# Performance work log

Hardware: AMD Instinct MI355X
Metric: run time of the kernel (lower is better)

The kernel has to match this reference:

```python
import jax, jax.numpy as jnp
import numpy as np

N_QUBITS = 12
N_LAYERS = 4


def rot_mat(phi, theta, omega):
    # PennyLane Rot(phi,theta,omega) = RZ(omega) @ RY(theta) @ RZ(phi)
    c = jnp.cos(theta / 2).astype(jnp.complex64)
    s = jnp.sin(theta / 2).astype(jnp.complex64)
    ep = jnp.exp(-1j * (phi + omega) / 2).astype(jnp.complex64)
    em = jnp.exp(1j * (phi - omega) / 2).astype(jnp.complex64)
    return jnp.stack([
        jnp.stack([ep * c, -em * s]),
        jnp.stack([jnp.conj(em) * s, jnp.conj(ep) * c]),
    ])  # (2,2) complex64


def apply_1q(state, U, w):
    # state: (batch, 2, 2, ..., 2) with N_QUBITS qubit axes
    s = jnp.moveaxis(state, w + 1, 1)
    s = jnp.einsum('ij,bj...->bi...', U, s)
    return jnp.moveaxis(s, 1, w + 1)


def apply_cnot(state, c, t):
    s = jnp.moveaxis(state, (c + 1, t + 1), (1, 2))
    s = jnp.concatenate([s[:, :1], s[:, 1:, ::-1]], axis=1)  # flip target where control=1
    return jnp.moveaxis(s, (1, 2), (c + 1, t + 1))


def setup_inputs() -> dict:
    key = jax.random.key(0)
    ks = jax.random.split(key, 6)
    L, F, n = 128, 96, N_QUBITS
    x = jax.random.normal(ks[0], (64, L, 32), dtype=jnp.float32)
    W_in = jax.random.normal(ks[1], (2 ** n, L), dtype=jnp.float32) * 0.05
    b_in = jax.random.normal(ks[2], (2 ** n,), dtype=jnp.float32) * 0.05
    q_weights = jax.random.uniform(ks[3], (N_LAYERS, n, 3), dtype=jnp.float32,
                                   minval=0.0, maxval=2.0 * np.pi)
    W_out = jax.random.normal(ks[4], (F, n), dtype=jnp.float32) * 0.1
    b_out = jax.random.normal(ks[5], (F,), dtype=jnp.float32) * 0.1
    return {"x": x, "W_in": W_in, "b_in": b_in, "q_weights": q_weights,
            "W_out": W_out, "b_out": b_out}


def reference(x, W_in, b_in, q_weights, W_out, b_out):
    n = N_QUBITS
    B, L, M = x.shape
    h = x.transpose(0, 2, 1).reshape(B * M, L)
    h = h @ W_in.T + b_in + 1e-6
    # AmplitudeEmbedding with normalize=True
    h = h / jnp.linalg.norm(h, axis=1, keepdims=True)
    state = h.astype(jnp.complex64).reshape((B * M,) + (2,) * n)
    # StronglyEntanglingLayers: per layer Rot on every wire, then CNOT ring with range r
    for l in range(N_LAYERS):
        for w in range(n):
            U = rot_mat(q_weights[l, w, 0], q_weights[l, w, 1], q_weights[l, w, 2])
            state = apply_1q(state, U, w)
        r = l % (n - 1) + 1
        for w in range(n):
            state = apply_cnot(state, w, (w + r) % n)
    probs = state.real ** 2 + state.imag ** 2  # (BM, 2,...,2)
    zs = []
    for i in range(n):
        axes = tuple(a for a in range(1, n + 1) if a != i + 1)
        p = probs.sum(axis=axes)  # (BM, 2)
        zs.append(p[:, 0] - p[:, 1])
    z = jnp.stack(zs, axis=1)  # (BM, n) expvals of PauliZ
    out = z @ W_out.T + b_out  # (BM, F)
    return out.reshape(B, M, -1).transpose(0, 2, 1)  # (B, F, M)
```

## Files before the change

### kernel.cpp

```cpp
#include <hip/hip_runtime.h>
#include <math.h>

#define NQ 12
#define DIM 4096
#define NSAMP 2048
#define NLAYERS 4

typedef _Float16 h8v __attribute__((ext_vector_type(8)));
typedef short s8v __attribute__((ext_vector_type(8)));
typedef float f4v __attribute__((ext_vector_type(4)));

struct QMasks { unsigned short mv[NLAYERS][12]; };

static void cnot_masks(int l, unsigned* m) {
    int r = l % (NQ - 1) + 1;
    for (int j = 0; j < NQ; ++j) {
        unsigned v = 1u << j;
        for (int k = NQ - 1; k >= 0; --k) {
            int c = k, t = (k + r) % NQ;
            int pc = NQ - 1 - c, pt = NQ - 1 - t;
            if ((v >> pc) & 1u) v ^= (1u << pt);
        }
        m[j] = v;
    }
}

static QMasks host_masks() {
    QMasks Q{};
    for (int l = 0; l < NLAYERS; ++l) {
        unsigned m[12];
        cnot_masks(l, m);
        unsigned A[12], I[12];
        for (int k = 0; k < 12; ++k) {
            unsigned row = 0;
            for (int j = 0; j < 12; ++j) row |= ((m[j] >> k) & 1u) << j;
            A[k] = row; I[k] = 1u << k;
        }
        for (int c = 0; c < 12; ++c) {
            int p = c; while (!((A[p] >> c) & 1u)) ++p;
            unsigned ta = A[p], ti = I[p]; A[p] = A[c]; I[p] = I[c]; A[c] = ta; I[c] = ti;
            for (int r2 = 0; r2 < 12; ++r2)
                if (r2 != c && ((A[r2] >> c) & 1u)) { A[r2] ^= A[c]; I[r2] ^= I[c]; }
        }
        for (int j = 0; j < 12; ++j) {
            unsigned colv = 0;
            for (int k = 0; k < 12; ++k) colv |= ((I[k] >> j) & 1u) << k;
            Q.mv[l][j] = (unsigned short)colv;
        }
    }
    return Q;
}

__device__ __forceinline__ unsigned short f2bf(float f) {
    unsigned u = __builtin_bit_cast(unsigned, f);
    return (unsigned short)((u + 0x7FFFu + ((u >> 16) & 1u)) >> 16);
}
__device__ __forceinline__ float bf2f(unsigned short b) {
    unsigned u = ((unsigned)b) << 16;
    return __builtin_bit_cast(float, u);
}
__device__ __forceinline__ unsigned packh(float re, float im) {
    unsigned short rb = __builtin_bit_cast(unsigned short, (_Float16)re);
    unsigned short ib = __builtin_bit_cast(unsigned short, (_Float16)im);
    return (unsigned)rb | ((unsigned)ib << 16);
}
__device__ __forceinline__ float h2f(unsigned short h) {
    return (float)__builtin_bit_cast(_Float16, h);
}

#define LDA 72
__global__ __launch_bounds__(256) void gemm_in_mfma(
        const float* __restrict__ x, const float* __restrict__ Win,
        const float* __restrict__ bin, const float* __restrict__ qw,
        unsigned short* __restrict__ h16, h8v* __restrict__ gates) {
    __shared__ unsigned short Ah[64 * LDA], Al[64 * LDA];
    __shared__ unsigned short Bh[64 * LDA], Bl[64 * LDA];
    const int tid = threadIdx.x;

    if (blockIdx.y == 32) {
        const int s = blockIdx.x;
        if (s >= 12 || tid >= 64) return;
        const int layer = s / 3, sg = s % 3;
        const int row = tid & 15, hi = tid >> 4;
        float ur[4][2][2], ui[4][2][2];
        for (int t = 0; t < 4; ++t) {
            const float* q = qw + (layer * NQ + sg * 4 + t) * 3;
            float sn, cs, sa, ca, sb, cb;
            sincosf(0.5f * q[1], &sn, &cs);
            sincosf(0.5f * (q[0] + q[2]), &sa, &ca);
            sincosf(0.5f * (q[0] - q[2]), &sb, &cb);
            ur[t][0][0] =  cs * ca; ui[t][0][0] = -cs * sa;
            ur[t][0][1] = -sn * cb; ui[t][0][1] = -sn * sb;
            ur[t][1][0] =  sn * cb; ui[t][1][0] = -sn * sb;
            ur[t][1][1] =  cs * ca; ui[t][1][1] =  cs * sa;
        }
        h8v arh, arl, aih, ail;
        for (int mm = 0; mm < 4; ++mm) {
            int m = hi * 4 + mm;
            float gr = 1.f, gi = 0.f;
            for (int t = 0; t < 4; ++t) {
                int rb = (row >> (3 - t)) & 1, cb2 = (m >> (3 - t)) & 1;
                float ar = ur[t][rb][cb2], ai = ui[t][rb][cb2];
                float nr = gr * ar - gi * ai, ni = gr * ai + gi * ar;
                gr = nr; gi = ni;
            }
            float vv[4] = {gr, -gi, gi, gr};
            _Float16 hh;
            hh = (_Float16)vv[0]; arh[2*mm]   = hh; arl[2*mm]   = (_Float16)(vv[0] - (float)hh);
            hh = (_Float16)vv[1]; arh[2*mm+1] = hh; arl[2*mm+1] = (_Float16)(vv[1] - (float)hh);
            hh = (_Float16)vv[2]; aih[2*mm]   = hh; ail[2*mm]   = (_Float16)(vv[2] - (float)hh);
            hh = (_Float16)vv[3]; aih[2*mm+1] = hh; ail[2*mm+1] = (_Float16)(vv[3] - (float)hh);
        }
        gates[(s * 4 + 0) * 64 + tid] = arh;
        gates[(s * 4 + 1) * 64 + tid] = arl;
        gates[(s * 4 + 2) * 64 + tid] = aih;
        gates[(s * 4 + 3) * 64 + tid] = ail;
        return;
    }

    const int kBase = blockIdx.x * 64;
    const int sBase = blockIdx.y * 64;
    const int lane = tid & 63, wid = tid >> 6;
    const int wr = wid >> 1, wc = wid & 1;
    const int l16 = lane & 15, lg = lane >> 4;
    const int xbase = (sBase >> 5) * 4096;
    f4v acc[2][2] = {};

#pragma unroll 1
    for (int ch = 0; ch < 2; ++ch) {
        __syncthreads();
#pragma unroll
        for (int it = 0; it < 4; ++it) {
            int idx = it * 256 + tid;
            int row = idx >> 4, c4 = (idx & 15) * 4;
            const float4 w = *(const float4*)&Win[(kBase + row) * 128 + ch * 64 + c4];
            ushort4 hi4, lo4;
            hi4.x = f2bf(w.x); lo4.x = f2bf(w.x - bf2f(hi4.x));
            hi4.y = f2bf(w.y); lo4.y = f2bf(w.y - bf2f(hi4.y));
            hi4.z = f2bf(w.z); lo4.z = f2bf(w.z - bf2f(hi4.z));
            hi4.w = f2bf(w.w); lo4.w = f2bf(w.w - bf2f(hi4.w));
            *(ushort4*)&Ah[row * LDA + c4] = hi4;
            *(ushort4*)&Al[row * LDA + c4] = lo4;
        }
#pragma unroll
        for (int it = 0; it < 16; ++it) {
            int idx = it * 256 + tid;
            int srow = idx & 63, l = idx >> 6;
            float val = x[xbase + (srow >> 5) * 4096 + (ch * 64 + l) * 32 + (srow & 31)];
            unsigned short hv = f2bf(val);
            Bh[srow * LDA + l] = hv;
            Bl[srow * LDA + l] = f2bf(val - bf2f(hv));
        }
        __syncthreads();
#pragma unroll
        for (int kk = 0; kk < 2; ++kk) {
            s8v ah[2], al2[2], bh[2], bl[2];
#pragma unroll
            for (int r = 0; r < 2; ++r) {
                int row = wr * 32 + r * 16 + l16;
                ah[r]  = *(s8v*)&Ah[row * LDA + kk * 32 + lg * 8];
                al2[r] = *(s8v*)&Al[row * LDA + kk * 32 + lg * 8];
            }
#pragma unroll
            for (int c = 0; c < 2; ++c) {
                int col = wc * 32 + c * 16 + l16;
                bh[c] = *(s8v*)&Bh[col * LDA + kk * 32 + lg * 8];
                bl[c] = *(s8v*)&Bl[col * LDA + kk * 32 + lg * 8];
            }
#pragma unroll
            for (int r = 0; r < 2; ++r)
#pragma unroll
                for (int c = 0; c < 2; ++c) {
                    acc[r][c] = __builtin_amdgcn_mfma_f32_16x16x32_bf16(ah[r],  bh[c], acc[r][c], 0, 0, 0);
                    acc[r][c] = __builtin_amdgcn_mfma_f32_16x16x32_bf16(ah[r],  bl[c], acc[r][c], 0, 0, 0);
                    acc[r][c] = __builtin_amdgcn_mfma_f32_16x16x32_bf16(al2[r], bh[c], acc[r][c], 0, 0, 0);
                }
        }
    }
#pragma unroll
    for (int r = 0; r < 2; ++r) {
        const int kg = kBase + wr * 32 + r * 16 + lg * 4;
        const float4 b4 = *(const float4*)&bin[kg];
#pragma unroll
        for (int c = 0; c < 2; ++c) {
            const int sg2 = sBase + wc * 32 + c * 16 + l16;
            ushort4 o;
            o.x = __builtin_bit_cast(unsigned short, (_Float16)(acc[r][c][0] + b4.x + 1e-6f));
            o.y = __builtin_bit_cast(unsigned short, (_Float16)(acc[r][c][1] + b4.y + 1e-6f));
            o.z = __builtin_bit_cast(unsigned short, (_Float16)(acc[r][c][2] + b4.z + 1e-6f));
            o.w = __builtin_bit_cast(unsigned short, (_Float16)(acc[r][c][3] + b4.w + 1e-6f));
            *(ushort4*)&h16[(size_t)sg2 * 4096 + kg] = o;
        }
    }
}

#define BUFW 4608

__global__ __launch_bounds__(256, 2) void qsim_mfma(
        const unsigned short* __restrict__ h16, const h8v* __restrict__ gates,
        const float* __restrict__ Wout, const float* __restrict__ bout,
        float* __restrict__ out, QMasks Q) {
    __shared__ unsigned lds[2 * BUFW];
    __shared__ float red[4];
    __shared__ float wred[4][13];
    __shared__ float zsh[13];

    const int tid = threadIdx.x;
    const int samp = blockIdx.x;
    const int lane = tid & 63;
    const int wv = tid >> 6;
    const int l16 = tid & 15;
    const int hi = (tid >> 4) & 3;
    const f4v fz = {0.f, 0.f, 0.f, 0.f};

    float vr[16]; float ss = 0.f;
#pragma unroll
    for (int j = 0; j < 16; ++j) {
        float f = h2f(h16[samp * DIM + j * 256 + tid]);
        vr[j] = f; ss += f * f;
    }
#pragma unroll
    for (int o = 32; o > 0; o >>= 1) ss += __shfl_xor(ss, o);
    if (lane == 0) red[wv] = ss;
    __syncthreads();
    const float inv = 1.0f / sqrtf(red[0] + red[1] + red[2] + red[3]);
#pragma unroll
    for (int j = 0; j < 16; ++j)
        lds[tid * 18 + j] = packh(vr[j] * inv, 0.f);
    __syncthreads();

    h8v ArH, ArL, AiH, AiL;
    f4v dre, dim_;

#define LOAD_FRAGS(S) { const h8v* gp = gates + (S) * 256 + lane;             \
    ArH = gp[0]; ArL = gp[64]; AiH = gp[128]; AiL = gp[192]; }

#define TILE_COMPUTE(RB, CG) {                                                \
    unsigned ra = (RB) + ((unsigned)(((CG) << 4) | l16)) * 18u + (hi << 2);   \
    uint2 w0 = *(const uint2*)&lds[ra];                                       \
    uint2 w1 = *(const uint2*)&lds[ra + 2];                                   \
    uint4 bw; bw.x = w0.x; bw.y = w0.y; bw.z = w1.x; bw.w = w1.y;             \
    h8v bf = __builtin_bit_cast(h8v, bw);                                     \
    dre = __builtin_amdgcn_mfma_f32_16x16x32_f16(ArH, bf, fz, 0, 0, 0);       \
    dre = __builtin_amdgcn_mfma_f32_16x16x32_f16(ArL, bf, dre, 0, 0, 0);      \
    dim_ = __builtin_amdgcn_mfma_f32_16x16x32_f16(AiH, bf, fz, 0, 0, 0);      \
    dim_ = __builtin_amdgcn_mfma_f32_16x16x32_f16(AiL, bf, dim_, 0, 0, 0); }

#define WRITE_S0(WB, CG) {                                                    \
    unsigned wa = (WB) + 1152u * hi + 18u * l16 + (unsigned)(CG);             \
    lds[wa]        = packh(dre[0], dim_[0]);                                  \
    lds[wa + 288]  = packh(dre[1], dim_[1]);                                  \
    lds[wa + 576]  = packh(dre[2], dim_[2]);                                  \
    lds[wa + 864]  = packh(dre[3], dim_[3]); }

#define WRITE_S1(WB, CG) {                                                    \
    unsigned wa = (WB) + 288u * (unsigned)(CG) + 72u * hi + (unsigned)l16;    \
    lds[wa]       = packh(dre[0], dim_[0]);                                   \
    lds[wa + 18]  = packh(dre[1], dim_[1]);                                   \
    lds[wa + 36]  = packh(dre[2], dim_[2]);                                   \
    lds[wa + 54]  = packh(dre[3], dim_[3]); }

#define RUN_LAYER(L, A, B)                                                    \
    LOAD_FRAGS(3 * (L) + 0)                                                   \
    { TILE_COMPUTE(A, 4 * wv + 0) WRITE_S0(B, 4 * wv + 0) }                   \
    { TILE_COMPUTE(A, 4 * wv + 1) WRITE_S0(B, 4 * wv + 1) }                   \
    { TILE_COMPUTE(A, 4 * wv + 2) WRITE_S0(B, 4 * wv + 2) }                   \
    { TILE_COMPUTE(A, 4 * wv + 3) WRITE_S0(B, 4 * wv + 3) }                   \
    __syncthreads();                                                          \
    LOAD_FRAGS(3 * (L) + 1)                                                   \
    { TILE_COMPUTE(B, 4 * wv + 0) WRITE_S1(A, 4 * wv + 0) }                   \
    { TILE_COMPUTE(B, 4 * wv + 1) WRITE_S1(A, 4 * wv + 1) }                   \
    { TILE_COMPUTE(B, 4 * wv + 2) WRITE_S1(A, 4 * wv + 2) }                   \
    { TILE_COMPUTE(B, 4 * wv + 3) WRITE_S1(A, 4 * wv + 3) }                   \
    __syncthreads();                                                          \
    LOAD_FRAGS(3 * (L) + 2)                                                   \
    {                                                                         \
        unsigned bb0 = 0;                                                     \
        if (hi & 1)  bb0 ^= Q.mv[L][2];  if (hi & 2)  bb0 ^= Q.mv[L][3];      \
        if (l16 & 1) bb0 ^= Q.mv[L][4];  if (l16 & 2) bb0 ^= Q.mv[L][5];      \
        if (l16 & 4) bb0 ^= Q.mv[L][6];  if (l16 & 8) bb0 ^= Q.mv[L][7];      \
        if (wv & 1)  bb0 ^= Q.mv[L][10]; if (wv & 2)  bb0 ^= Q.mv[L][11];     \
        _Pragma("unroll")                                                     \
        for (int T = 0; T < 4; ++T) {                                         \
            TILE_COMPUTE(A, 4 * wv + T)                                       \
            unsigned bb = bb0;                                                \
            if (T & 1) bb ^= Q.mv[L][8];                                      \
            if (T & 2) bb ^= Q.mv[L][9];                                      \
            unsigned b0 = bb;                                                 \
            unsigned b1 = bb ^ Q.mv[L][0];                                    \
            unsigned b2 = bb ^ Q.mv[L][1];                                    \
            unsigned b3 = b1 ^ Q.mv[L][1];                                    \
            lds[(B) + (b0 & 255u) * 18u + (b0 >> 8)] = packh(dre[0], dim_[0]); \
            lds[(B) + (b1 & 255u) * 18u + (b1 >> 8)] = packh(dre[1], dim_[1]); \
            lds[(B) + (b2 & 255u) * 18u + (b2 >> 8)] = packh(dre[2], dim_[2]); \
            lds[(B) + (b3 & 255u) * 18u + (b3 >> 8)] = packh(dre[3], dim_[3]); \
        }                                                                     \
    }                                                                         \
    __syncthreads();

    RUN_LAYER(0, 0, BUFW)
    RUN_LAYER(1, BUFW, 0)
    RUN_LAYER(2, 0, BUFW)
    RUN_LAYER(3, BUFW, 0)

    float P = 0.f;
    float z03[4] = {0.f, 0.f, 0.f, 0.f};
#pragma unroll
    for (int j = 0; j < 16; ++j) {
        unsigned w = lds[tid * 18 + j];
        float re = h2f((unsigned short)(w & 0xFFFFu));
        float im = h2f((unsigned short)(w >> 16));
        float pr = re * re + im * im;
        P += pr;
#pragma unroll
        for (int i = 0; i < 4; ++i)
            z03[i] += ((j >> (3 - i)) & 1) ? -pr : pr;
    }
    float zv[12];
#pragma unroll
    for (int i = 0; i < 4; ++i) zv[i] = z03[i];
#pragma unroll
    for (int i = 4; i < 12; ++i)
        zv[i] = ((tid >> (11 - i)) & 1) ? -P : P;
#pragma unroll
    for (int i = 0; i < 12; ++i) {
        float z = zv[i];
#pragma unroll
        for (int o = 32; o > 0; o >>= 1) z += __shfl_xor(z, o);
        if (lane == 0) wred[wv][i] = z;
    }
    {
        float v = P;
#pragma unroll
        for (int o = 32; o > 0; o >>= 1) v += __shfl_xor(v, o);
        if (lane == 0) wred[wv][12] = v;
    }
    __syncthreads();
    if (tid < 13)
        zsh[tid] = wred[0][tid] + wred[1][tid] + wred[2][tid] + wred[3][tid];
    __syncthreads();

    if (tid < 96) {
        const float invP = 1.0f / zsh[12];
        float acc = bout[tid];
#pragma unroll
        for (int i = 0; i < 12; ++i) acc += zsh[i] * invP * Wout[tid * 12 + i];
        int b = samp >> 5, m = samp & 31;
        out[b * (96 * 32) + tid * 32 + m] = acc;
    }
}

extern "C" void kernel_launch(void* const* d_in, const int* in_sizes, int n_in,
                              void* d_out, int out_size, void* d_ws, size_t ws_size,
                              hipStream_t stream) {
    const float* x    = (const float*)d_in[0];
    const float* Win  = (const float*)d_in[1];
    const float* bin  = (const float*)d_in[2];
    const float* qw   = (const float*)d_in[3];
    const float* Wout = (const float*)d_in[4];
    const float* bout = (const float*)d_in[5];
    unsigned short* h16 = (unsigned short*)d_ws;
    h8v* gates = (h8v*)((char*)d_ws + (size_t)NSAMP * DIM * 2);

    QMasks Q = host_masks();

    gemm_in_mfma<<<dim3(64, 33), 256, 0, stream>>>(x, Win, bin, qw, h16, gates);
    qsim_mfma<<<dim3(NSAMP), 256, 0, stream>>>(h16, gates, Wout, bout,
                                               (float*)d_out, Q);
}
```

Baseline: 75.22 us.

## Use single in-place LDS buffer with stride 20 and raise occupancy to 4 blocks

Replaces the double-buffered LDS state (two 4608-word buffers) with a single 256x20 buffer. All four tiles are computed into registers, then a barrier, then written back in place. The padded stride of 20 allows 128-bit LDS loads and vectorized uint4 stores for the first stage, and launch bounds rise to 4 blocks per CU. This halves LDS use so more blocks fit per CU, at the cost of an extra barrier per stage, more live accumulator registers, and possibly different bank-conflict behaviour.

```diff
diff --git a/kernel.cpp b/kernel.cpp
--- a/kernel.cpp
+++ b/kernel.cpp
@@ -194,13 +194,13 @@
     }
 }
 
-#define BUFW 4608
-
-__global__ __launch_bounds__(256, 2) void qsim_mfma(
+#define ST 20u
+
+__global__ __launch_bounds__(256, 4) void qsim_mfma(
         const unsigned short* __restrict__ h16, const h8v* __restrict__ gates,
         const float* __restrict__ Wout, const float* __restrict__ bout,
         float* __restrict__ out, QMasks Q) {
-    __shared__ unsigned lds[2 * BUFW];
+    __shared__ __align__(16) unsigned lds[256 * 20];
     __shared__ float red[4];
     __shared__ float wred[4][13];
     __shared__ float zsh[13];
@@ -225,89 +225,89 @@
     __syncthreads();
     const float inv = 1.0f / sqrtf(red[0] + red[1] + red[2] + red[3]);
 #pragma unroll
-    for (int j = 0; j < 16; ++j)
-        lds[tid * 18 + j] = packh(vr[j] * inv, 0.f);
+    for (int q = 0; q < 4; ++q) {
+        uint4 w;
+        w.x = packh(vr[4 * q + 0] * inv, 0.f);
+        w.y = packh(vr[4 * q + 1] * inv, 0.f);
+        w.z = packh(vr[4 * q + 2] * inv, 0.f);
+        w.w = packh(vr[4 * q + 3] * inv, 0.f);
+        *(uint4*)&lds[tid * ST + 4 * q] = w;
+    }
     __syncthreads();
 
     h8v ArH, ArL, AiH, AiL;
-    f4v dre, dim_;
+    f4v dre0, dre1, dre2, dre3, dim0, dim1, dim2, dim3;
 
 #define LOAD_FRAGS(S) { const h8v* gp = gates + (S) * 256 + lane;             \
     ArH = gp[0]; ArL = gp[64]; AiH = gp[128]; AiL = gp[192]; }
 
-#define TILE_COMPUTE(RB, CG) {                                                \
-    unsigned ra = (RB) + ((unsigned)(((CG) << 4) | l16)) * 18u + (hi << 2);   \
-    uint2 w0 = *(const uint2*)&lds[ra];                                       \
-    uint2 w1 = *(const uint2*)&lds[ra + 2];                                   \
-    uint4 bw; bw.x = w0.x; bw.y = w0.y; bw.z = w1.x; bw.w = w1.y;             \
-    h8v bf = __builtin_bit_cast(h8v, bw);                                     \
-    dre = __builtin_amdgcn_mfma_f32_16x16x32_f16(ArH, bf, fz, 0, 0, 0);       \
-    dre = __builtin_amdgcn_mfma_f32_16x16x32_f16(ArL, bf, dre, 0, 0, 0);      \
-    dim_ = __builtin_amdgcn_mfma_f32_16x16x32_f16(AiH, bf, fz, 0, 0, 0);      \
-    dim_ = __builtin_amdgcn_mfma_f32_16x16x32_f16(AiL, bf, dim_, 0, 0, 0); }
-
-#define WRITE_S0(WB, CG) {                                                    \
-    unsigned wa = (WB) + 1152u * hi + 18u * l16 + (unsigned)(CG);             \
-    lds[wa]        = packh(dre[0], dim_[0]);                                  \
-    lds[wa + 288]  = packh(dre[1], dim_[1]);                                  \
-    lds[wa + 576]  = packh(dre[2], dim_[2]);                                  \
-    lds[wa + 864]  = packh(dre[3], dim_[3]); }
-
-#define WRITE_S1(WB, CG) {                                                    \
-    unsigned wa = (WB) + 288u * (unsigned)(CG) + 72u * hi + (unsigned)l16;    \
-    lds[wa]       = packh(dre[0], dim_[0]);                                   \
-    lds[wa + 18]  = packh(dre[1], dim_[1]);                                   \
-    lds[wa + 36]  = packh(dre[2], dim_[2]);                                   \
-    lds[wa + 54]  = packh(dre[3], dim_[3]); }
-
-#define RUN_LAYER(L, A, B)                                                    \
-    LOAD_FRAGS(3 * (L) + 0)                                                   \
-    { TILE_COMPUTE(A, 4 * wv + 0) WRITE_S0(B, 4 * wv + 0) }                   \
-    { TILE_COMPUTE(A, 4 * wv + 1) WRITE_S0(B, 4 * wv + 1) }                   \
-    { TILE_COMPUTE(A, 4 * wv + 2) WRITE_S0(B, 4 * wv + 2) }                   \
-    { TILE_COMPUTE(A, 4 * wv + 3) WRITE_S0(B, 4 * wv + 3) }                   \
-    __syncthreads();                                                          \
-    LOAD_FRAGS(3 * (L) + 1)                                                   \
-    { TILE_COMPUTE(B, 4 * wv + 0) WRITE_S1(A, 4 * wv + 0) }                   \
-    { TILE_COMPUTE(B, 4 * wv + 1) WRITE_S1(A, 4 * wv + 1) }                   \
-    { TILE_COMPUTE(B, 4 * wv + 2) WRITE_S1(A, 4 * wv + 2) }                   \
-    { TILE_COMPUTE(B, 4 * wv + 3) WRITE_S1(A, 4 * wv + 3) }                   \
-    __syncthreads();                                                          \
-    LOAD_FRAGS(3 * (L) + 2)                                                   \
-    {                                                                         \
-        unsigned bb0 = 0;                                                     \
-        if (hi & 1)  bb0 ^= Q.mv[L][2];  if (hi & 2)  bb0 ^= Q.mv[L][3];      \
-        if (l16 & 1) bb0 ^= Q.mv[L][4];  if (l16 & 2) bb0 ^= Q.mv[L][5];      \
-        if (l16 & 4) bb0 ^= Q.mv[L][6];  if (l16 & 8) bb0 ^= Q.mv[L][7];      \
-        if (wv & 1)  bb0 ^= Q.mv[L][10]; if (wv & 2)  bb0 ^= Q.mv[L][11];     \
-        _Pragma("unroll")                                                     \
-        for (int T = 0; T < 4; ++T) {                                         \
-            TILE_COMPUTE(A, 4 * wv + T)                                       \
-            unsigned bb = bb0;                                                \
-            if (T & 1) bb ^= Q.mv[L][8];                                      \
-            if (T & 2) bb ^= Q.mv[L][9];                                      \
-            unsigned b0 = bb;                                                 \
-            unsigned b1 = bb ^ Q.mv[L][0];                                    \
-            unsigned b2 = bb ^ Q.mv[L][1];                                    \
-            unsigned b3 = b1 ^ Q.mv[L][1];                                    \
-            lds[(B) + (b0 & 255u) * 18u + (b0 >> 8)] = packh(dre[0], dim_[0]); \
-            lds[(B) + (b1 & 255u) * 18u + (b1 >> 8)] = packh(dre[1], dim_[1]); \
-            lds[(B) + (b2 & 255u) * 18u + (b2 >> 8)] = packh(dre[2], dim_[2]); \
-            lds[(B) + (b3 & 255u) * 18u + (b3 >> 8)] = packh(dre[3], dim_[3]); \
-        }                                                                     \
-    }                                                                         \
-    __syncthreads();
-
-    RUN_LAYER(0, 0, BUFW)
-    RUN_LAYER(1, BUFW, 0)
-    RUN_LAYER(2, 0, BUFW)
-    RUN_LAYER(3, BUFW, 0)
+#define TC(T, DRE, DIM) {                                                     \
+    unsigned ra = ((unsigned)(((4 * wv + (T)) << 4) | l16)) * ST + (unsigned)(hi << 2); \
+    h8v bf = __builtin_bit_cast(h8v, *(const uint4*)&lds[ra]);                \
+    DRE = __builtin_amdgcn_mfma_f32_16x16x32_f16(ArH, bf, fz, 0, 0, 0);       \
+    DRE = __builtin_amdgcn_mfma_f32_16x16x32_f16(ArL, bf, DRE, 0, 0, 0);      \
+    DIM = __builtin_amdgcn_mfma_f32_16x16x32_f16(AiH, bf, fz, 0, 0, 0);       \
+    DIM = __builtin_amdgcn_mfma_f32_16x16x32_f16(AiL, bf, DIM, 0, 0, 0); }
+
+#define COMPUTE4                                                              \
+    TC(0, dre0, dim0) TC(1, dre1, dim1) TC(2, dre2, dim2) TC(3, dre3, dim3)   \
+    __syncthreads();
+
+#define WS0REG(R, OFF) {                                                      \
+    uint4 w;                                                                  \
+    w.x = packh(dre0[R], dim0[R]); w.y = packh(dre1[R], dim1[R]);             \
+    w.z = packh(dre2[R], dim2[R]); w.w = packh(dre3[R], dim3[R]);             \
+    *(uint4*)&lds[wb0 + (OFF)] = w; }
+#define WS0 {                                                                 \
+    unsigned wb0 = 1280u * hi + ST * (unsigned)l16 + 4u * wv;                 \
+    WS0REG(0, 0) WS0REG(1, 320) WS0REG(2, 640) WS0REG(3, 960) }               \
+    __syncthreads();
+
+#define WS1T(T, DRE, DIM) {                                                   \
+    unsigned wa = 320u * (unsigned)(4 * wv + (T)) + 80u * hi + (unsigned)l16; \
+    lds[wa]      = packh(DRE[0], DIM[0]);                                     \
+    lds[wa + 20] = packh(DRE[1], DIM[1]);                                     \
+    lds[wa + 40] = packh(DRE[2], DIM[2]);                                     \
+    lds[wa + 60] = packh(DRE[3], DIM[3]); }
+#define WS1 { WS1T(0, dre0, dim0) WS1T(1, dre1, dim1)                         \
+              WS1T(2, dre2, dim2) WS1T(3, dre3, dim3) }                       \
+    __syncthreads();
+
+#define X3T(L, T, DRE, DIM) {                                                 \
+    unsigned bb = bb0;                                                        \
+    if ((T) & 1) bb ^= Q.mv[L][8];                                            \
+    if ((T) & 2) bb ^= Q.mv[L][9];                                            \
+    unsigned b0 = bb, b1 = bb ^ Q.mv[L][0];                                   \
+    unsigned b2 = bb ^ Q.mv[L][1], b3 = b1 ^ Q.mv[L][1];                      \
+    lds[(b0 & 255u) * ST + (b0 >> 8)] = packh(DRE[0], DIM[0]);                \
+    lds[(b1 & 255u) * ST + (b1 >> 8)] = packh(DRE[1], DIM[1]);                \
+    lds[(b2 & 255u) * ST + (b2 >> 8)] = packh(DRE[2], DIM[2]);                \
+    lds[(b3 & 255u) * ST + (b3 >> 8)] = packh(DRE[3], DIM[3]); }
+#define WX3(L) {                                                              \
+    unsigned bb0 = 0;                                                         \
+    if (hi & 1)  bb0 ^= Q.mv[L][2];  if (hi & 2)  bb0 ^= Q.mv[L][3];          \
+    if (l16 & 1) bb0 ^= Q.mv[L][4];  if (l16 & 2) bb0 ^= Q.mv[L][5];          \
+    if (l16 & 4) bb0 ^= Q.mv[L][6];  if (l16 & 8) bb0 ^= Q.mv[L][7];          \
+    if (wv & 1)  bb0 ^= Q.mv[L][10]; if (wv & 2)  bb0 ^= Q.mv[L][11];         \
+    X3T(L, 0, dre0, dim0) X3T(L, 1, dre1, dim1)                               \
+    X3T(L, 2, dre2, dim2) X3T(L, 3, dre3, dim3) }                             \
+    __syncthreads();
+
+#define RUN_LAYER(L)                                                          \
+    LOAD_FRAGS(3 * (L) + 0) COMPUTE4 WS0                                      \
+    LOAD_FRAGS(3 * (L) + 1) COMPUTE4 WS1                                      \
+    LOAD_FRAGS(3 * (L) + 2) COMPUTE4 WX3(L)
+
+    RUN_LAYER(0)
+    RUN_LAYER(1)
+    RUN_LAYER(2)
+    RUN_LAYER(3)
 
     float P = 0.f;
     float z03[4] = {0.f, 0.f, 0.f, 0.f};
 #pragma unroll
     for (int j = 0; j < 16; ++j) {
-        unsigned w = lds[tid * 18 + j];
+        unsigned w = lds[tid * ST + j];
         float re = h2f((unsigned short)(w & 0xFFFFu));
         float im = h2f((unsigned short)(w >> 16));
         float pr = re * re + im * im;
```

Measured after the change: 77.04 us. 1.02x slower.
